# Performance work log

Hardware: AMD Instinct MI355X
Metric: run time of the kernel (lower is better)

## Reference

```python
import jax, jax.numpy as jnp
import numpy as np

DIM = 256      # model/channel dim (== dim_inner)
DT_RANK = 16   # low-rank dt projection
D_STATE = 16   # SSM state size N
BATCH = 4
SEQLEN = 4096


def setup_inputs() -> dict:
    key = jax.random.key(0)
    ks = jax.random.split(key, 8)
    s = 1.0 / np.sqrt(DIM)
    x = jax.random.normal(ks[0], (BATCH, SEQLEN, DIM), jnp.float32)
    W_proj = jax.random.normal(ks[1], (DIM, DIM), jnp.float32) * s
    b_proj = jax.random.normal(ks[2], (DIM,), jnp.float32) * s
    conv_w = jax.random.normal(ks[3], (DIM, 3), jnp.float32) * 0.3   # depthwise kernel, taps [t-1, t, t+1]
    conv_b = jnp.zeros((DIM,), jnp.float32)
    W_dbc = jax.random.normal(ks[4], (DIM, DT_RANK + 2 * D_STATE), jnp.float32) * s  # -> [delta_lowrank | B | C]
    W_dt = jax.random.normal(ks[5], (DT_RANK, DIM), jnp.float32) / np.sqrt(DT_RANK)
    b_dt = jax.random.normal(ks[6], (DIM,), jnp.float32) * 0.1
    A_log = jnp.log(jnp.broadcast_to(jnp.arange(1, D_STATE + 1, dtype=jnp.float32), (DIM, D_STATE)))
    D_skip = jnp.ones((DIM,), jnp.float32)
    return dict(x=x, W_proj=W_proj, b_proj=b_proj, conv_w=conv_w, conv_b=conv_b,
                W_dbc=W_dbc, W_dt=W_dt, b_dt=b_dt, A_log=A_log, D_skip=D_skip)


def reference(x, W_proj, b_proj, conv_w, conv_b, W_dbc, W_dt, b_dt, A_log, D_skip):
    skip = x
    x_one = x @ W_proj + b_proj            # (B,L,D)
    x_two = x @ W_proj + b_proj            # same (single) linear, per the module's prof/proj
    # depthwise Conv1d(kernel=3, padding=1, groups=D) over the sequence axis
    xp = jnp.pad(x_one, ((0, 0), (1, 1), (0, 0)))
    x_one = (xp[:, :-2] * conv_w[:, 0] + xp[:, 1:-1] * conv_w[:, 1]
             + xp[:, 2:] * conv_w[:, 2]) + conv_b
    x_one = jax.nn.silu(x_one)
    # --- selective-scan SSM ---
    A = -jnp.exp(A_log)                    # (D,N)
    dbc = x_one @ W_dbc                    # (B,L,DT+2N)
    delta, Bm, Cm = jnp.split(dbc, [DT_RANK, DT_RANK + D_STATE], axis=-1)
    delta = jax.nn.softplus(delta @ W_dt + b_dt)                 # (B,L,D)
    deltaA = jnp.exp(delta[..., None] * A)                       # (B,L,D,N)
    deltaBX = delta[..., None] * Bm[:, :, None, :] * x_one[..., None]  # (B,L,D,N)

    def step(h, ab):
        a_t, b_t = ab
        h = a_t * h + b_t
        return h, h

    h0 = jnp.zeros((x.shape[0], DIM, D_STATE), x.dtype)
    _, hs = jax.lax.scan(step, h0, (deltaA.swapaxes(0, 1), deltaBX.swapaxes(0, 1)))
    hs = hs.swapaxes(0, 1)                                       # (B,L,D,N)
    y = jnp.einsum('bldn,bln->bld', hs, Cm) + D_skip * x_one     # SSM output
    # gated residual
    out = y * jax.nn.silu(x_two) + skip
    return out @ W_proj + b_proj
```

## Files before the change

### kernel.cpp

```cpp
#include <hip/hip_runtime.h>
#include <math.h>

#define B_ 4
#define L_ 4096
#define D_ 256
#define N_ 16
#define DTR 16
#define NC 128
#define LC 32
#define M_ (B_*L_)

typedef __attribute__((ext_vector_type(8))) short short8;
typedef __attribute__((ext_vector_type(4))) float floatx4;

__device__ __forceinline__ float silu_f(float v) { return v / (1.f + __expf(-v)); }

__device__ __forceinline__ unsigned short f2bf(float f) {
  union { float f; unsigned u; } v; v.f = f;
  unsigned r = (v.u + 0x7FFFu + ((v.u >> 16) & 1u)) >> 16;
  return (unsigned short)r;
}
__device__ __forceinline__ float bf2f(unsigned short s) {
  union { unsigned u; float f; } v; v.u = (unsigned)s << 16; return v.f;
}
__device__ __forceinline__ float bflo(unsigned u) {
  union { unsigned u; float f; } v; v.u = u << 16; return v.f;
}
__device__ __forceinline__ float bfhi(unsigned u) {
  union { unsigned u; float f; } v; v.u = u & 0xFFFF0000u; return v.f;
}

__device__ __forceinline__ float softplus_f(float x) {
  return fmaxf(x, 0.f) + __logf(1.f + __expf(-fabsf(x)));
}

__global__ __launch_bounds__(256) void convert_w_k(
    const float* __restrict__ W, const float* __restrict__ Wdbc,
    unsigned short* __restrict__ Wt, unsigned short* __restrict__ Wdbct)
{
  const int k = blockIdx.x;
  const int n = threadIdx.x;
  Wt[n * 256 + k] = f2bf(W[k * 256 + n]);
  if (n < 48) Wdbct[n * 256 + k] = f2bf(Wdbc[k * 48 + n]);
}

__global__ __launch_bounds__(512) void conv_all_k(
    const float* __restrict__ x, const float* __restrict__ conv_w,
    const float* __restrict__ conv_b, const unsigned short* __restrict__ Wt,
    const unsigned short* __restrict__ Wdbct,
    const float* __restrict__ Wdt, const float* __restrict__ bdt,
    const float* __restrict__ A_log, const float* __restrict__ bias,
    unsigned short* __restrict__ lin16, unsigned* __restrict__ dxc,
    float* __restrict__ Bm, float* __restrict__ Cm,
    float* __restrict__ Pp, float* __restrict__ Sp)
{
  __shared__ __align__(16) char smA[25344];
  __shared__ __align__(16) char smB[25344];
  unsigned short (*xsa)[264]  = (unsigned short(*)[264])smA;
  unsigned short (*xcb)[264]  = (unsigned short(*)[264])smA;
  float (*dlow)[17] = (float(*)[17])(smA + 16896);
  float (*Bsh)[17]  = (float(*)[17])(smA + 16896 + 2176);
  unsigned short (*linb)[264] = (unsigned short(*)[264])smB;
  unsigned short (*dlt)[264]  = (unsigned short(*)[264])smB;

  const int blk = blockIdx.x;
  const int b  = blk >> 7;
  const int c  = blk & (NC - 1);
  const int l0 = c * LC;
  const int tid = threadIdx.x;
  const int lane = tid & 63, w = tid >> 6;
  const int l15 = lane & 15, lg = lane >> 4;
  const int kk = lg * 8;

  for (int q = tid; q < 48 * 64; q += 512) {
    const int row = q >> 6, f4 = (q & 63) * 4;
    int g = b * L_ + l0 - 8 + row;
    g = g < 0 ? 0 : (g >= M_ ? M_ - 1 : g);
    const float4 v = *(const float4*)(x + (size_t)g * 256 + f4);
    ushort4 bv;
    bv.x = f2bf(v.x); bv.y = f2bf(v.y); bv.z = f2bf(v.z); bv.w = f2bf(v.w);
    *(ushort4*)&xsa[row][f4] = bv;
  }
  __syncthreads();

  {
    const int c0w = w * 32;
    floatx4 acc[3][2];
    #pragma unroll
    for (int rg = 0; rg < 3; ++rg)
      #pragma unroll
      for (int f = 0; f < 2; ++f) acc[rg][f] = (floatx4){0.f, 0.f, 0.f, 0.f};
    #pragma unroll
    for (int ks = 0; ks < 8; ++ks) {
      const short8 af0 = *(const short8*)&xsa[ 0 + l15][ks * 32 + kk];
      const short8 af1 = *(const short8*)&xsa[16 + l15][ks * 32 + kk];
      const short8 af2 = *(const short8*)&xsa[32 + l15][ks * 32 + kk];
      #pragma unroll
      for (int f = 0; f < 2; ++f) {
        const short8 bf_ = *(const short8*)(Wt + (c0w + f * 16 + l15) * 256 + ks * 32 + kk);
        acc[0][f] = __builtin_amdgcn_mfma_f32_16x16x32_bf16(af0, bf_, acc[0][f], 0, 0, 0);
        acc[1][f] = __builtin_amdgcn_mfma_f32_16x16x32_bf16(af1, bf_, acc[1][f], 0, 0, 0);
        acc[2][f] = __builtin_amdgcn_mfma_f32_16x16x32_bf16(af2, bf_, acc[2][f], 0, 0, 0);
      }
    }
    __syncthreads();
    #pragma unroll
    for (int rg = 0; rg < 3; ++rg)
      #pragma unroll
      for (int f = 0; f < 2; ++f) {
        const int col = c0w + f * 16 + l15;
        const float bb = bias[col];
        #pragma unroll
        for (int r = 0; r < 4; ++r)
          linb[rg * 16 + lg * 4 + r][col] = f2bf(acc[rg][f][r] + bb);
      }
  }
  __syncthreads();

  for (int q = tid; q < 32 * 64; q += 512) {
    const int r = q >> 6, dq = (q & 63) * 4;
    const int l = l0 + r;
    const int lr = r + 8;
    const ushort4 z = {0, 0, 0, 0};
    const ushort4 c0u = (l > 0)      ? *(const ushort4*)&linb[lr - 1][dq] : z;
    const ushort4 c1u = *(const ushort4*)&linb[lr][dq];
    const ushort4 c2u = (l < L_ - 1) ? *(const ushort4*)&linb[lr + 1][dq] : z;
    *(ushort4*)(lin16 + (size_t)(b * L_ + l) * D_ + dq) = c1u;
    float4 v;
    v.x = silu_f(bf2f(c0u.x)*conv_w[(dq+0)*3+0] + bf2f(c1u.x)*conv_w[(dq+0)*3+1] + bf2f(c2u.x)*conv_w[(dq+0)*3+2] + conv_b[dq+0]);
    v.y = silu_f(bf2f(c0u.y)*conv_w[(dq+1)*3+0] + bf2f(c1u.y)*conv_w[(dq+1)*3+1] + bf2f(c2u.y)*conv_w[(dq+1)*3+2] + conv_b[dq+1]);
    v.z = silu_f(bf2f(c0u.z)*conv_w[(dq+2)*3+0] + bf2f(c1u.z)*conv_w[(dq+2)*3+1] + bf2f(c2u.z)*conv_w[(dq+2)*3+2] + conv_b[dq+2]);
    v.w = silu_f(bf2f(c0u.w)*conv_w[(dq+3)*3+0] + bf2f(c1u.w)*conv_w[(dq+3)*3+1] + bf2f(c2u.w)*conv_w[(dq+3)*3+2] + conv_b[dq+3]);
    ushort4 bv;
    bv.x = f2bf(v.x); bv.y = f2bf(v.y); bv.z = f2bf(v.z); bv.w = f2bf(v.w);
    *(ushort4*)&xcb[r][dq] = bv;
  }
  __syncthreads();

  if (w < 2) {
    const int arow = w * 16 + l15;
    floatx4 acc[3];
    #pragma unroll
    for (int nt = 0; nt < 3; ++nt) acc[nt] = (floatx4){0.f, 0.f, 0.f, 0.f};
    #pragma unroll
    for (int ks = 0; ks < 8; ++ks) {
      const short8 af = *(const short8*)&xcb[arow][ks * 32 + kk];
      #pragma unroll
      for (int nt = 0; nt < 3; ++nt) {
        const short8 bf_ = *(const short8*)(Wdbct + (nt * 16 + l15) * 256 + ks * 32 + kk);
        acc[nt] = __builtin_amdgcn_mfma_f32_16x16x32_bf16(af, bf_, acc[nt], 0, 0, 0);
      }
    }
    const int row = w * 16 + lg * 4;
    const int gl = (b * L_ + l0 + row) * N_ + l15;
    #pragma unroll
    for (int r = 0; r < 4; ++r) {
      dlow[row + r][l15]   = acc[0][r];
      Bsh[row + r][l15]    = acc[1][r];
      Bm[gl + r * N_]      = acc[1][r];
      Cm[gl + r * N_]      = acc[2][r];
    }
  }
  __syncthreads();

  for (int q = tid; q < 32 * 64; q += 512) {
    const int r = q >> 6, dq = (q & 63) * 4;
    float4 s = *(const float4*)(bdt + dq);
    #pragma unroll
    for (int k = 0; k < DTR; ++k) {
      const float f = dlow[r][k];
      const float4 wv = *(const float4*)(Wdt + k * D_ + dq);
      s.x = fmaf(f, wv.x, s.x); s.y = fmaf(f, wv.y, s.y);
      s.z = fmaf(f, wv.z, s.z); s.w = fmaf(f, wv.w, s.w);
    }
    ushort4 dv;
    dv.x = f2bf(softplus_f(s.x)); dv.y = f2bf(softplus_f(s.y));
    dv.z = f2bf(softplus_f(s.z)); dv.w = f2bf(softplus_f(s.w));
    *(ushort4*)&dlt[r][dq] = dv;
    uint4 o;
    o.x = (unsigned)dv.x | ((unsigned)xcb[r][dq + 0] << 16);
    o.y = (unsigned)dv.y | ((unsigned)xcb[r][dq + 1] << 16);
    o.z = (unsigned)dv.z | ((unsigned)xcb[r][dq + 2] << 16);
    o.w = (unsigned)dv.w | ((unsigned)xcb[r][dq + 3] << 16);
    *(uint4*)(dxc + (size_t)(b * L_ + (l0 + r)) * D_ + dq) = o;
  }
  __syncthreads();

  {
    const int nh = tid & 1, d = tid >> 1, n0 = nh * 8;
    float A[8], P[8], S[8];
    bool fast = true;
    #pragma unroll
    for (int n = 0; n < 8; ++n) {
      A[n] = -__expf(A_log[d * N_ + n0 + n]);
      const float k = (float)(n0 + n + 1);
      fast = fast && (fabsf(A[n] + k) < 1e-3f * k);
      P[n] = 1.f; S[n] = 0.f;
    }
    if (fast) {
      float sumdv = 0.f;
      for (int t = 0; t < LC; ++t) {
        const float dv = bf2f(dlt[t][d]);
        const float xv = bf2f(xcb[t][d]);
        const float dvx = dv * xv;
        const float rr = __expf(-dv);
        sumdv += dv;
        float a;
        if (nh) { const float r2 = rr * rr, r4 = r2 * r2; a = r4 * r4 * rr; }
        else    a = rr;
        #pragma unroll
        for (int n = 0; n < 8; ++n) {
          S[n] = fmaf(a, S[n], dvx * Bsh[t][n0 + n]);
          a *= rr;
        }
      }
      const float R = __expf(-sumdv);
      float pr;
      if (nh) { const float R2 = R * R, R4 = R2 * R2; pr = R4 * R4 * R; }
      else    pr = R;
      #pragma unroll
      for (int n = 0; n < 8; ++n) { P[n] = pr; pr *= R; }
    } else {
      for (int t = 0; t < LC; ++t) {
        const float dv = bf2f(dlt[t][d]);
        const float xv = bf2f(xcb[t][d]);
        const float dvx = dv * xv;
        #pragma unroll
        for (int n = 0; n < 8; ++n) {
          const float a = __expf(dv * A[n]);
          S[n] = fmaf(a, S[n], dvx * Bsh[t][n0 + n]);
          P[n] *= a;
        }
      }
    }
    const int o = ((b * D_ + d) * NC + c) * N_ + n0;
    *(float4*)(Pp + o)     = *(const float4*)&P[0];
    *(float4*)(Pp + o + 4) = *(const float4*)&P[4];
    *(float4*)(Sp + o)     = *(const float4*)&S[0];
    *(float4*)(Sp + o + 4) = *(const float4*)&S[4];
  }
}

__global__ __launch_bounds__(128) void scan_pass2_k(
    const float* Pp, const float* Sp, float* Hin)
{
  __shared__ float lP[N_][NC + 1];
  __shared__ float lS[N_][NC + 1];
  const int bd = blockIdx.x;
  const int c = threadIdx.x;
  const int base = bd * NC * N_ + c * N_;
  float P[N_], S[N_];
  #pragma unroll
  for (int q = 0; q < 4; ++q) {
    *(float4*)&P[q * 4] = *(const float4*)(Pp + base + q * 4);
    *(float4*)&S[q * 4] = *(const float4*)(Sp + base + q * 4);
  }
  #pragma unroll
  for (int n = 0; n < N_; ++n) { lP[n][c] = P[n]; lS[n][c] = S[n]; }
  for (int s = 1; s < NC; s <<= 1) {
    __syncthreads();
    float Pb[N_], Sb[N_];
    if (c >= s) {
      #pragma unroll
      for (int n = 0; n < N_; ++n) { Pb[n] = lP[n][c - s]; Sb[n] = lS[n][c - s]; }
    }
    __syncthreads();
    if (c >= s) {
      #pragma unroll
      for (int n = 0; n < N_; ++n) {
        S[n] = fmaf(P[n], Sb[n], S[n]);
        P[n] *= Pb[n];
        lP[n][c] = P[n]; lS[n][c] = S[n];
      }
    }
  }
  __syncthreads();
  float h[N_];
  if (c == 0) {
    #pragma unroll
    for (int n = 0; n < N_; ++n) h[n] = 0.f;
  } else {
    #pragma unroll
    for (int n = 0; n < N_; ++n) h[n] = lS[n][c - 1];
  }
  #pragma unroll
  for (int q = 0; q < 4; ++q)
    *(float4*)(Hin + base + q * 4) = *(const float4*)&h[q * 4];
}

__global__ __launch_bounds__(512) void scan3_gemm2_k(
    const unsigned* __restrict__ dxc,
    const float* __restrict__ Bm, const float* __restrict__ Cm,
    const float* __restrict__ A_log, const float* __restrict__ Dskip,
    const float* __restrict__ Hin, const unsigned short* __restrict__ lin16,
    const float* __restrict__ xin, const unsigned short* __restrict__ Wt,
    const float* __restrict__ bias, float* __restrict__ out)
{
  __shared__ unsigned short Asl[32][264];
  __shared__ unsigned short Wsl[256][40];
  __shared__ float Bs[LC][N_];
  __shared__ float Cs[LC][N_];
  const int blk = blockIdx.x;
  const int b = blk >> 7, c = blk & (NC - 1);
  const int tid = threadIdx.x;
  const int row0 = blk * 32;

  {
    const int src = (b * L_ + c * LC) * N_ + tid;
    Bs[tid >> 4][tid & 15] = Bm[src];
    Cs[tid >> 4][tid & 15] = Cm[src];
  }
  __syncthreads();

  {
    const int nh = tid & 1, d = tid >> 1, n0 = nh * 8;
    const float dsk = Dskip[d];
    float A[8], h[8];
    bool fast = true;
    const int ho = ((b * D_ + d) * NC + c) * N_ + n0;
    #pragma unroll
    for (int n = 0; n < 8; ++n) {
      A[n] = -__expf(A_log[d * N_ + n0 + n]);
      const float k = (float)(n0 + n + 1);
      fast = fast && (fabsf(A[n] + k) < 1e-3f * k);
    }
    *(float4*)&h[0] = *(const float4*)(Hin + ho);
    *(float4*)&h[4] = *(const float4*)(Hin + ho + 4);
    int base = (b * L_ + c * LC) * D_ + d;
    unsigned u = dxc[base];
    if (fast) {
      #pragma unroll 4
      for (int t = 0; t < LC; ++t) {
        const unsigned u_n = (t < LC - 1) ? dxc[base + D_] : 0u;
        const float dv = bflo(u), xv = bfhi(u);
        const float dvx = dv * xv;
        float bv[8], cv[8];
        *(float4*)&bv[0] = *(const float4*)&Bs[t][n0];
        *(float4*)&bv[4] = *(const float4*)&Bs[t][n0 + 4];
        *(float4*)&cv[0] = *(const float4*)&Cs[t][n0];
        *(float4*)&cv[4] = *(const float4*)&Cs[t][n0 + 4];
        const float r = __expf(-dv);
        float a;
        if (nh) { const float r2 = r * r, r4 = r2 * r2; a = r4 * r4 * r; }
        else    a = r;
        float p = 0.f;
        #pragma unroll
        for (int n = 0; n < 8; ++n) {
          h[n] = fmaf(a, h[n], dvx * bv[n]);
          p = fmaf(h[n], cv[n], p);
          a *= r;
        }
        p += __shfl_xor(p, 1);
        if (nh == 0) Asl[t][d] = f2bf(fmaf(dsk, xv, p));
        u = u_n; base += D_;
      }
    } else {
      for (int t = 0; t < LC; ++t) {
        const unsigned uu = dxc[base];
        const float dvv = bflo(uu);
        const float xvv = bfhi(uu);
        const float dvx = dvv * xvv;
        float bv[8], cv[8];
        *(float4*)&bv[0] = *(const float4*)&Bs[t][n0];
        *(float4*)&bv[4] = *(const float4*)&Bs[t][n0 + 4];
        *(float4*)&cv[0] = *(const float4*)&Cs[t][n0];
        *(float4*)&cv[4] = *(const float4*)&Cs[t][n0 + 4];
        float p = 0.f;
        #pragma unroll
        for (int n = 0; n < 8; ++n) {
          const float a = __expf(dvv * A[n]);
          h[n] = fmaf(a, h[n], dvx * bv[n]);
          p = fmaf(h[n], cv[n], p);
        }
        p += __shfl_xor(p, 1);
        if (nh == 0) Asl[t][d] = f2bf(fmaf(dsk, xvv, p));
        base += D_;
      }
    }
  }
  __syncthreads();

  for (int q = tid; q < 32 * 64; q += 512) {
    const int r = q >> 6, dq = (q & 63) * 4;
    const int off = (row0 + r) * 256 + dq;
    const ushort4 lv = *(const ushort4*)(lin16 + off);
    const float4  xv = *(const float4*)(xin + off);
    ushort4 yv = *(const ushort4*)&Asl[r][dq];
    ushort4 av;
    av.x = f2bf(fmaf(bf2f(yv.x), silu_f(bf2f(lv.x)), xv.x));
    av.y = f2bf(fmaf(bf2f(yv.y), silu_f(bf2f(lv.y)), xv.y));
    av.z = f2bf(fmaf(bf2f(yv.z), silu_f(bf2f(lv.z)), xv.z));
    av.w = f2bf(fmaf(bf2f(yv.w), silu_f(bf2f(lv.w)), xv.w));
    *(ushort4*)&Asl[r][dq] = av;
  }

  const int lane = tid & 63, w = tid >> 6;
  const int l15 = lane & 15, lg = lane >> 4;
  const int arow = (w & 1) * 16 + l15;
  const int ctile = (w >> 1) * 64;
  const int kk = lg * 8;
  const int wn = tid >> 1, wkc = (tid & 1) * 16;
  floatx4 acc[4];
  #pragma unroll
  for (int f = 0; f < 4; ++f) acc[f] = (floatx4){0.f, 0.f, 0.f, 0.f};

  for (int ks = 0; ks < 8; ++ks) {
    __syncthreads();
    *(uint4*)&Wsl[wn][wkc + 0] = *(const uint4*)(Wt + wn * 256 + ks * 32 + wkc);
    *(uint4*)&Wsl[wn][wkc + 8] = *(const uint4*)(Wt + wn * 256 + ks * 32 + wkc + 8);
    __syncthreads();
    const short8 af = *(const short8*)&Asl[arow][ks * 32 + kk];
    #pragma unroll
    for (int f = 0; f < 4; ++f) {
      const short8 bf_ = *(const short8*)&Wsl[ctile + f * 16 + l15][kk];
      acc[f] = __builtin_amdgcn_mfma_f32_16x16x32_bf16(af, bf_, acc[f], 0, 0, 0);
    }
  }
  const int growb = row0 + (w & 1) * 16 + lg * 4;
  #pragma unroll
  for (int f = 0; f < 4; ++f) {
    const int col = ctile + f * 16 + l15;
    const float bb = bias[col];
    #pragma unroll
    for (int r = 0; r < 4; ++r)
      out[(growb + r) * 256 + col] = acc[f][r] + bb;
  }
}

extern "C" void kernel_launch(void* const* d_in, const int* in_sizes, int n_in,
                              void* d_out, int out_size, void* d_ws, size_t ws_size,
                              hipStream_t stream) {
  const float* x      = (const float*)d_in[0];
  const float* W_proj = (const float*)d_in[1];
  const float* b_proj = (const float*)d_in[2];
  const float* conv_w = (const float*)d_in[3];
  const float* conv_b = (const float*)d_in[4];
  const float* W_dbc  = (const float*)d_in[5];
  const float* W_dt   = (const float*)d_in[6];
  const float* b_dt   = (const float*)d_in[7];
  const float* A_log  = (const float*)d_in[8];
  const float* D_skip = (const float*)d_in[9];
  float* out = (float*)d_out;

  float* ws    = (float*)d_ws;
  const size_t SZ = (size_t)M_ * D_;
  const size_t PSZ = (size_t)B_ * D_ * NC * N_;
  unsigned short* lin16 = (unsigned short*)ws;
  unsigned* dxc = (unsigned*)(ws + SZ);
  float*    Pp  = ws + 2 * SZ;
  float*    Sp  = Pp + PSZ;
  float*    Hin = Pp;
  float*    Bm  = ws + 3 * SZ;
  float*    Cm  = Bm + (size_t)M_ * N_;
  unsigned short* Wt    = (unsigned short*)(Cm + (size_t)M_ * N_);
  unsigned short* Wdbct = Wt + 256 * 256;

  convert_w_k<<<dim3(256), dim3(256), 0, stream>>>(W_proj, W_dbc, Wt, Wdbct);
  conv_all_k<<<dim3(512), dim3(512), 0, stream>>>(
      x, conv_w, conv_b, Wt, Wdbct, W_dt, b_dt, A_log, b_proj,
      lin16, dxc, Bm, Cm, Pp, Sp);
  scan_pass2_k<<<dim3(1024), dim3(128), 0, stream>>>(Pp, Sp, Hin);
  scan3_gemm2_k<<<dim3(512), dim3(512), 0, stream>>>(
      dxc, Bm, Cm, A_log, D_skip, Hin, lin16, x, Wt, b_proj, out);
}
```

Baseline: 79.70 us.

## Halve conv/scan-pass1 chunk length to double block count

```diff
diff --git a/kernel.cpp b/kernel.cpp
--- a/kernel.cpp
+++ b/kernel.cpp
@@ -8,6 +8,8 @@
 #define DTR 16
 #define NC 128
 #define LC 32
+#define NCH 256
+#define LCH 16
 #define M_ (B_*L_)
 
 typedef __attribute__((ext_vector_type(8))) short short8;
@@ -54,25 +56,25 @@
     float* __restrict__ Bm, float* __restrict__ Cm,
     float* __restrict__ Pp, float* __restrict__ Sp)
 {
-  __shared__ __align__(16) char smA[25344];
-  __shared__ __align__(16) char smB[25344];
+  __shared__ __align__(16) char smA[16896];
+  __shared__ __align__(16) char smB[16896];
   unsigned short (*xsa)[264]  = (unsigned short(*)[264])smA;
   unsigned short (*xcb)[264]  = (unsigned short(*)[264])smA;
-  float (*dlow)[17] = (float(*)[17])(smA + 16896);
-  float (*Bsh)[17]  = (float(*)[17])(smA + 16896 + 2176);
+  float (*dlow)[17] = (float(*)[17])(smA + 8448);
+  float (*Bsh)[17]  = (float(*)[17])(smA + 8448 + 1088);
   unsigned short (*linb)[264] = (unsigned short(*)[264])smB;
   unsigned short (*dlt)[264]  = (unsigned short(*)[264])smB;
 
   const int blk = blockIdx.x;
-  const int b  = blk >> 7;
-  const int c  = blk & (NC - 1);
-  const int l0 = c * LC;
+  const int b  = blk >> 8;
+  const int ch = blk & (NCH - 1);
+  const int l0 = ch * LCH;
   const int tid = threadIdx.x;
   const int lane = tid & 63, w = tid >> 6;
   const int l15 = lane & 15, lg = lane >> 4;
   const int kk = lg * 8;
 
-  for (int q = tid; q < 48 * 64; q += 512) {
+  for (int q = tid; q < 32 * 64; q += 512) {
     const int row = q >> 6, f4 = (q & 63) * 4;
     int g = b * L_ + l0 - 8 + row;
     g = g < 0 ? 0 : (g >= M_ ? M_ - 1 : g);
@@ -85,27 +87,25 @@
 
   {
     const int c0w = w * 32;
-    floatx4 acc[3][2];
-    #pragma unroll
-    for (int rg = 0; rg < 3; ++rg)
+    floatx4 acc[2][2];
+    #pragma unroll
+    for (int rg = 0; rg < 2; ++rg)
       #pragma unroll
       for (int f = 0; f < 2; ++f) acc[rg][f] = (floatx4){0.f, 0.f, 0.f, 0.f};
     #pragma unroll
     for (int ks = 0; ks < 8; ++ks) {
       const short8 af0 = *(const short8*)&xsa[ 0 + l15][ks * 32 + kk];
       const short8 af1 = *(const short8*)&xsa[16 + l15][ks * 32 + kk];
-      const short8 af2 = *(const short8*)&xsa[32 + l15][ks * 32 + kk];
       #pragma unroll
       for (int f = 0; f < 2; ++f) {
         const short8 bf_ = *(const short8*)(Wt + (c0w + f * 16 + l15) * 256 + ks * 32 + kk);
         acc[0][f] = __builtin_amdgcn_mfma_f32_16x16x32_bf16(af0, bf_, acc[0][f], 0, 0, 0);
         acc[1][f] = __builtin_amdgcn_mfma_f32_16x16x32_bf16(af1, bf_, acc[1][f], 0, 0, 0);
-        acc[2][f] = __builtin_amdgcn_mfma_f32_16x16x32_bf16(af2, bf_, acc[2][f], 0, 0, 0);
       }
     }
     __syncthreads();
     #pragma unroll
-    for (int rg = 0; rg < 3; ++rg)
+    for (int rg = 0; rg < 2; ++rg)
       #pragma unroll
       for (int f = 0; f < 2; ++f) {
         const int col = c0w + f * 16 + l15;
@@ -117,7 +117,7 @@
   }
   __syncthreads();
 
-  for (int q = tid; q < 32 * 64; q += 512) {
+  for (int q = tid; q < 16 * 64; q += 512) {
     const int r = q >> 6, dq = (q & 63) * 4;
     const int l = l0 + r;
     const int lr = r + 8;
@@ -137,21 +137,20 @@
   }
   __syncthreads();
 
-  if (w < 2) {
-    const int arow = w * 16 + l15;
+  if (w == 0) {
     floatx4 acc[3];
     #pragma unroll
     for (int nt = 0; nt < 3; ++nt) acc[nt] = (floatx4){0.f, 0.f, 0.f, 0.f};
     #pragma unroll
     for (int ks = 0; ks < 8; ++ks) {
-      const short8 af = *(const short8*)&xcb[arow][ks * 32 + kk];
+      const short8 af = *(const short8*)&xcb[l15][ks * 32 + kk];
       #pragma unroll
       for (int nt = 0; nt < 3; ++nt) {
         const short8 bf_ = *(const short8*)(Wdbct + (nt * 16 + l15) * 256 + ks * 32 + kk);
         acc[nt] = __builtin_amdgcn_mfma_f32_16x16x32_bf16(af, bf_, acc[nt], 0, 0, 0);
       }
     }
-    const int row = w * 16 + lg * 4;
+    const int row = lg * 4;
     const int gl = (b * L_ + l0 + row) * N_ + l15;
     #pragma unroll
     for (int r = 0; r < 4; ++r) {
@@ -163,7 +162,7 @@
   }
   __syncthreads();
 
-  for (int q = tid; q < 32 * 64; q += 512) {
+  for (int q = tid; q < 16 * 64; q += 512) {
     const int r = q >> 6, dq = (q & 63) * 4;
     float4 s = *(const float4*)(bdt + dq);
     #pragma unroll
@@ -199,7 +198,7 @@
     }
     if (fast) {
       float sumdv = 0.f;
-      for (int t = 0; t < LC; ++t) {
+      for (int t = 0; t < LCH; ++t) {
         const float dv = bf2f(dlt[t][d]);
         const float xv = bf2f(xcb[t][d]);
         const float dvx = dv * xv;
@@ -221,7 +220,7 @@
       #pragma unroll
       for (int n = 0; n < 8; ++n) { P[n] = pr; pr *= R; }
     } else {
-      for (int t = 0; t < LC; ++t) {
+      for (int t = 0; t < LCH; ++t) {
         const float dv = bf2f(dlt[t][d]);
         const float xv = bf2f(xcb[t][d]);
         const float dvx = dv * xv;
@@ -233,7 +232,7 @@
         }
       }
     }
-    const int o = ((b * D_ + d) * NC + c) * N_ + n0;
+    const int o = ((b * D_ + d) * NCH + ch) * N_ + n0;
     *(float4*)(Pp + o)     = *(const float4*)&P[0];
     *(float4*)(Pp + o + 4) = *(const float4*)&P[4];
     *(float4*)(Sp + o)     = *(const float4*)&S[0];
@@ -241,14 +240,14 @@
   }
 }
 
-__global__ __launch_bounds__(128) void scan_pass2_k(
+__global__ __launch_bounds__(256) void scan_pass2_k(
     const float* Pp, const float* Sp, float* Hin)
 {
-  __shared__ float lP[N_][NC + 1];
-  __shared__ float lS[N_][NC + 1];
+  __shared__ float lP[N_][NCH + 1];
+  __shared__ float lS[N_][NCH + 1];
   const int bd = blockIdx.x;
   const int c = threadIdx.x;
-  const int base = bd * NC * N_ + c * N_;
+  const int base = bd * NCH * N_ + c * N_;
   float P[N_], S[N_];
   #pragma unroll
   for (int q = 0; q < 4; ++q) {
@@ -257,7 +256,7 @@
   }
   #pragma unroll
   for (int n = 0; n < N_; ++n) { lP[n][c] = P[n]; lS[n][c] = S[n]; }
-  for (int s = 1; s < NC; s <<= 1) {
+  for (int s = 1; s < NCH; s <<= 1) {
     __syncthreads();
     float Pb[N_], Sb[N_];
     if (c >= s) {
@@ -317,7 +316,7 @@
     const float dsk = Dskip[d];
     float A[8], h[8];
     bool fast = true;
-    const int ho = ((b * D_ + d) * NC + c) * N_ + n0;
+    const int ho = ((b * D_ + d) * NCH + 2 * c) * N_ + n0;
     #pragma unroll
     for (int n = 0; n < 8; ++n) {
       A[n] = -__expf(A_log[d * N_ + n0 + n]);
@@ -444,22 +443,21 @@
 
   float* ws    = (float*)d_ws;
   const size_t SZ = (size_t)M_ * D_;
-  const size_t PSZ = (size_t)B_ * D_ * NC * N_;
   unsigned short* lin16 = (unsigned short*)ws;
   unsigned* dxc = (unsigned*)(ws + SZ);
   float*    Pp  = ws + 2 * SZ;
-  float*    Sp  = Pp + PSZ;
+  float*    Sp  = ws + 3 * SZ;
   float*    Hin = Pp;
-  float*    Bm  = ws + 3 * SZ;
+  float*    Bm  = ws + 4 * SZ;
   float*    Cm  = Bm + (size_t)M_ * N_;
   unsigned short* Wt    = (unsigned short*)(Cm + (size_t)M_ * N_);
   unsigned short* Wdbct = Wt + 256 * 256;
 
   convert_w_k<<<dim3(256), dim3(256), 0, stream>>>(W_proj, W_dbc, Wt, Wdbct);
-  conv_all_k<<<dim3(512), dim3(512), 0, stream>>>(
+  conv_all_k<<<dim3(B_ * NCH), dim3(512), 0, stream>>>(
       x, conv_w, conv_b, Wt, Wdbct, W_dt, b_dt, A_log, b_proj,
       lin16, dxc, Bm, Cm, Pp, Sp);
-  scan_pass2_k<<<dim3(1024), dim3(128), 0, stream>>>(Pp, Sp, Hin);
+  scan_pass2_k<<<dim3(B_ * D_), dim3(256), 0, stream>>>(Pp, Sp, Hin);
   scan3_gemm2_k<<<dim3(512), dim3(512), 0, stream>>>(
       dxc, Bm, Cm, A_log, D_skip, Hin, lin16, x, Wt, b_proj, out);
 }
```

Result: slower. 97.22 us (+22.0%).
